# Performance work log

Hardware: AMD Instinct MI355X
Metric: run time of the kernel (lower is better)

Reference implementation:

```python
import jax, jax.numpy as jnp
from jax import lax
import numpy as np

N_TOTAL = 262144
NUM_SAMPLE = 1024
KNN_K = 16
NUM_CLASSES = 13
HIDDEN = 128
EPS = 1e-8


def _sqdist(a, b):
    # (Na,3),(Nb,3) -> (Na,Nb) squared euclidean; same argmin as torch.cdist
    return (jnp.sum(a * a, axis=1)[:, None]
            + jnp.sum(b * b, axis=1)[None, :]
            - 2.0 * a @ b.T)


def _farthest_point_sample(xyz, n_samples):
    # sequential FPS starting from index 0 (deterministic start)
    n = xyz.shape[0]

    def step(carry, _):
        min_d2, last = carry
        d2 = jnp.sum((xyz - xyz[last]) ** 2, axis=-1)
        min_d2 = jnp.minimum(min_d2, d2)
        nxt = jnp.argmax(min_d2).astype(jnp.int32)
        return (min_d2, nxt), nxt

    init = (jnp.full((n,), 1e10, dtype=xyz.dtype), jnp.int32(0))
    _, idxs = lax.scan(step, init, None, length=n_samples - 1)
    return jnp.concatenate([jnp.zeros((1,), jnp.int32), idxs])


def _compute_normals(pts, k):
    # PCA normal per point from its k nearest neighbors (self excluded)
    d2 = _sqdist(pts, pts)                      # (S,S), S=1024 -> small
    _, nbr_idx = lax.top_k(-d2, k + 1)
    nbr = pts[nbr_idx[:, 1:]]                   # (S,k,3)
    centered = nbr - jnp.mean(nbr, axis=1, keepdims=True)
    cov = jnp.einsum('ski,skj->sij', centered, centered) / (k - 1)
    _, eigvecs = jnp.linalg.eigh(cov)           # ascending eigenvalues
    normal = eigvecs[..., 0]                    # smallest-eigval eigenvector
    return normal / (jnp.linalg.norm(normal, axis=-1, keepdims=True) + EPS)


def _forward(gaussian_positions, gaussian_colors, W1, b1, W2, b2, W3, b3):
    sample_idx = _farthest_point_sample(gaussian_positions, NUM_SAMPLE)
    dxyz = gaussian_positions[sample_idx]       # (S,3)
    drgb = gaussian_colors[sample_idx]          # (S,3)
    dnrm = _compute_normals(dxyz, KNN_K)        # (S,3)
    feats = jnp.concatenate([dxyz, drgb, dnrm], axis=1)  # (S,9)

    # pointwise segmentation network (stand-in for PointNet++ get_model)
    h = jax.nn.relu(feats @ W1 + b1)
    h = jax.nn.relu(h @ W2 + b2)
    pred = h @ W3 + b3                          # (S, num_classes)

    feat_down = jax.nn.softmax(pred, axis=1)
    lbl_down = jnp.argmax(pred, axis=1)

    # 1-NN label propagation: streaming-min candidate (memory-bound)
    d2_full = _sqdist(gaussian_positions, dxyz)  # (N, S) ~ 1 GB
    nearest = jnp.argmin(d2_full, axis=1)
    return feat_down[nearest], lbl_down[nearest]


def setup_inputs() -> dict:
    key = jax.random.key(0)
    ks = jax.random.split(key, 8)
    pos = jax.random.normal(ks[0], (N_TOTAL, 3), jnp.float32)
    col = jax.random.uniform(ks[1], (N_TOTAL, 3), jnp.float32)
    W1 = jax.random.normal(ks[2], (9, HIDDEN), jnp.float32) / np.sqrt(9.0)
    b1 = jnp.zeros((HIDDEN,), jnp.float32)
    W2 = jax.random.normal(ks[3], (HIDDEN, HIDDEN), jnp.float32) / np.sqrt(HIDDEN)
    b2 = jnp.zeros((HIDDEN,), jnp.float32)
    W3 = jax.random.normal(ks[4], (HIDDEN, NUM_CLASSES), jnp.float32) / np.sqrt(HIDDEN)
    b3 = jnp.zeros((NUM_CLASSES,), jnp.float32)
    return {"gaussian_positions": pos, "gaussian_colors": col,
            "W1": W1, "b1": b1, "W2": W2, "b2": b2, "W3": W3, "b3": b3}


def reference(gaussian_positions, gaussian_colors, W1, b1, W2, b2, W3, b3):
    return _forward(gaussian_positions, gaussian_colors, W1, b1, W2, b2, W3, b3)
```

## Files before the change

### kernel.cpp

```cpp
#include <hip/hip_runtime.h>
#include <math.h>

#define N_TOTAL    262144
#define NUM_SAMPLE 1024
#define FPS_BLOCKS 64
#define FPS_THREADS 256
#define FPS_PPT (N_TOTAL / (FPS_BLOCKS * FPS_THREADS))
#define M_WAVE 8
#define POOL (FPS_BLOCKS * 4 * M_WAVE)
#define ENT_PER_T (POOL / FPS_THREADS)
#define SEL_CAP 1023

__device__ __forceinline__ float addrn(float a, float b) { return __fadd_rn(a, b); }
__device__ __forceinline__ float subrn(float a, float b) { return __fsub_rn(a, b); }
__device__ __forceinline__ float mulrn(float a, float b) { return __fmul_rn(a, b); }

__device__ __forceinline__ float d2rn(float ax, float ay, float az,
                                      float bx, float by, float bz) {
  float dx = subrn(ax, bx), dy = subrn(ay, by), dz = subrn(az, bz);
  return addrn(addrn(mulrn(dx, dx), mulrn(dy, dy)), mulrn(dz, dz));
}

__device__ __forceinline__ unsigned long long shflxor_u64(unsigned long long v, int mk) {
  return (unsigned long long)__shfl_xor((long long)v, mk, 64);
}

__device__ __forceinline__ float slapy2f(float x, float y) {
  float xa = fabsf(x), ya = fabsf(y);
  float w = fmaxf(xa, ya), z = fminf(xa, ya);
  if (z == 0.f) return w;
  float t = z / w;
  return w * __fsqrt_rn(1.f + t * t);
}

__device__ __forceinline__ void slartgf(float f, float g, float& c, float& s, float& r) {
  if (g == 0.f) { c = 1.f; s = 0.f; r = f; }
  else if (f == 0.f) { c = 0.f; s = (g > 0.f) ? 1.f : -1.f; r = fabsf(g); }
  else {
    float d = __fsqrt_rn(f * f + g * g);
    c = fabsf(f) / d;
    r = (f >= 0.f) ? d : -d;
    s = g / r;
  }
}

__device__ void slaev2f(float a, float b, float c0, float& rt1, float& rt2,
                        float& cs1, float& sn1) {
  float sm = a + c0, df = a - c0;
  float adf = fabsf(df), tb = b + b, ab = fabsf(tb);
  float acmx, acmn;
  if (fabsf(a) > fabsf(c0)) { acmx = a; acmn = c0; } else { acmx = c0; acmn = a; }
  float rt;
  if (adf > ab)      { float t = ab / adf; rt = adf * __fsqrt_rn(1.f + t * t); }
  else if (adf < ab) { float t = adf / ab; rt = ab * __fsqrt_rn(1.f + t * t); }
  else               { rt = ab * __fsqrt_rn(2.f); }
  int sgn1;
  if (sm < 0.f)      { rt1 = 0.5f * (sm - rt); sgn1 = -1; rt2 = (acmx / rt1) * acmn - (b / rt1) * b; }
  else if (sm > 0.f) { rt1 = 0.5f * (sm + rt); sgn1 = 1;  rt2 = (acmx / rt1) * acmn - (b / rt1) * b; }
  else               { rt1 = 0.5f * rt; rt2 = -0.5f * rt; sgn1 = 1; }
  float cs; int sgn2;
  if (df >= 0.f) { cs = df + rt; sgn2 = 1; } else { cs = df - rt; sgn2 = -1; }
  float acs = fabsf(cs);
  if (acs > ab) {
    float ct = -tb / cs;
    sn1 = 1.f / __fsqrt_rn(1.f + ct * ct);
    cs1 = ct * sn1;
  } else {
    if (ab == 0.f) { cs1 = 1.f; sn1 = 0.f; }
    else { float tn = -cs / tb; cs1 = 1.f / __fsqrt_rn(1.f + tn * tn); sn1 = tn * cs1; }
  }
  if (sgn1 == sgn2) { float tn = cs1; cs1 = -sn1; sn1 = tn; }
}

#define D_(i) d[(i)-1]
#define E_(i) e[(i)-1]

__device__ void ssteqr3(float d[3], float e[2], float Z[3][3]) {
  const float eps    = 5.9604645e-08f;
  const float eps2   = 3.5527137e-15f;
  const float safmin = 1.17549435e-38f;
  const float ssfmax = 3.0744573e+18f;
  const float ssfmin = 3.0517578e-05f;
  const int n = 3;
  int jtot = 0, nmaxit = 90;
  int l1 = 1;

  while (true) {
    if (l1 > n) break;
    if (l1 > 1) E_(l1 - 1) = 0.f;
    int m = n;
    for (int mm = l1; mm <= n - 1; ++mm) {
      float tst = fabsf(E_(mm));
      if (tst == 0.f) { m = mm; break; }
      if (tst <= (__fsqrt_rn(fabsf(D_(mm))) * __fsqrt_rn(fabsf(D_(mm + 1)))) * eps) {
        E_(mm) = 0.f; m = mm; break;
      }
    }
    int l = l1, lsv = l, lend = m, lendsv = m;
    l1 = m + 1;
    if (lend == l) continue;

    float anorm = fabsf(D_(lend));
    for (int i2 = l; i2 <= lend - 1; ++i2) {
      anorm = fmaxf(anorm, fabsf(D_(i2)));
      anorm = fmaxf(anorm, fabsf(E_(i2)));
    }
    int iscale = 0;
    if (anorm == 0.f) continue;
    if (anorm > ssfmax) {
      iscale = 1; float mul = ssfmax / anorm;
      for (int i2 = l; i2 <= lend; ++i2) D_(i2) *= mul;
      for (int i2 = l; i2 <= lend - 1; ++i2) E_(i2) *= mul;
    } else if (anorm < ssfmin) {
      iscale = 2; float mul = ssfmin / anorm;
      for (int i2 = l; i2 <= lend; ++i2) D_(i2) *= mul;
      for (int i2 = l; i2 <= lend - 1; ++i2) E_(i2) *= mul;
    }

    if (fabsf(D_(lend)) < fabsf(D_(l))) { int t = l; l = lend; lend = t; }

    if (lend > l) {
      while (true) {
        int m2 = lend;
        if (l != lend) {
          for (int mm = l; mm <= lend - 1; ++mm) {
            float tst = fabsf(E_(mm)); tst = tst * tst;
            if (tst <= (eps2 * fabsf(D_(mm))) * fabsf(D_(mm + 1)) + safmin) { m2 = mm; break; }
          }
        }
        if (m2 < lend) E_(m2) = 0.f;
        float p = D_(l);
        if (m2 == l) { D_(l) = p; l = l + 1; if (l <= lend) continue; break; }
        if (m2 == l + 1) {
          float rt1, rt2, cc, ss;
          slaev2f(D_(l), E_(l), D_(l + 1), rt1, rt2, cc, ss);
          for (int i2 = 0; i2 < 3; ++i2) {
            float tmp = Z[i2][l];
            Z[i2][l]     = cc * tmp - ss * Z[i2][l - 1];
            Z[i2][l - 1] = ss * tmp + cc * Z[i2][l - 1];
          }
          D_(l) = rt1; D_(l + 1) = rt2; E_(l) = 0.f;
          l = l + 2; if (l <= lend) continue; break;
        }
        if (jtot == nmaxit) break;
        ++jtot;
        float g = (D_(l + 1) - p) / (2.f * E_(l));
        float r = slapy2f(g, 1.f);
        float sgn_rg = (g >= 0.f) ? r : -r;
        g = D_(m2) - p + E_(l) / (g + sgn_rg);
        float s = 1.f, c = 1.f;
        p = 0.f;
        float csv[2], ssv[2];
        for (int i2 = m2 - 1; i2 >= l; --i2) {
          float f = s * E_(i2);
          float b = c * E_(i2);
          slartgf(g, f, c, s, r);
          if (i2 != m2 - 1) E_(i2 + 1) = r;
          g = D_(i2 + 1) - p;
          r = (D_(i2) - g) * s + 2.f * c * b;
          p = s * r;
          D_(i2 + 1) = g + p;
          g = c * r - b;
          csv[i2 - l] = c; ssv[i2 - l] = -s;
        }
        for (int j = m2 - 1; j >= l; --j) {
          float ct = csv[j - l], st = ssv[j - l];
          for (int i2 = 0; i2 < 3; ++i2) {
            float tmp = Z[i2][j];
            Z[i2][j]     = ct * tmp - st * Z[i2][j - 1];
            Z[i2][j - 1] = st * tmp + ct * Z[i2][j - 1];
          }
        }
        D_(l) = D_(l) - p;
        E_(l) = g;
      }
    } else {
      while (true) {
        int m2 = lend;
        if (l != lend) {
          for (int mm = l; mm >= lend + 1; --mm) {
            float tst = fabsf(E_(mm - 1)); tst = tst * tst;
            if (tst <= (eps2 * fabsf(D_(mm))) * fabsf(D_(mm - 1)) + safmin) { m2 = mm; break; }
          }
        }
        if (m2 > lend) E_(m2 - 1) = 0.f;
        float p = D_(l);
        if (m2 == l) { D_(l) = p; l = l - 1; if (l >= lend) continue; break; }
        if (m2 == l - 1) {
          float rt1, rt2, cc, ss;
          slaev2f(D_(l - 1), E_(l - 1), D_(l), rt1, rt2, cc, ss);
          for (int i2 = 0; i2 < 3; ++i2) {
            float tmp = Z[i2][l - 1];
            Z[i2][l - 1] = cc * tmp - ss * Z[i2][l - 2];
            Z[i2][l - 2] = ss * tmp + cc * Z[i2][l - 2];
          }
          D_(l - 1) = rt1; D_(l) = rt2; E_(l - 1) = 0.f;
          l = l - 2; if (l >= lend) continue; break;
        }
        if (jtot == nmaxit) break;
        ++jtot;
        float g = (D_(l - 1) - p) / (2.f * E_(l - 1));
        float r = slapy2f(g, 1.f);
        float sgn_rg = (g >= 0.f) ? r : -r;
        g = D_(m2) - p + E_(l - 1) / (g + sgn_rg);
        float s = 1.f, c = 1.f;
        p = 0.f;
        float csv[2], ssv[2];
        for (int i2 = m2; i2 <= l - 1; ++i2) {
          float f = s * E_(i2);
          float b = c * E_(i2);
          slartgf(g, f, c, s, r);
          if (i2 != m2) E_(i2 - 1) = r;
          g = D_(i2) - p;
          r = (D_(i2 + 1) - g) * s + 2.f * c * b;
          p = s * r;
          D_(i2) = g + p;
          g = c * r - b;
          csv[i2 - m2] = c; ssv[i2 - m2] = s;
        }
        for (int j = m2; j <= l - 1; ++j) {
          float ct = csv[j - m2], st = ssv[j - m2];
          for (int i2 = 0; i2 < 3; ++i2) {
            float tmp = Z[i2][j];
            Z[i2][j]     = ct * tmp - st * Z[i2][j - 1];
            Z[i2][j - 1] = st * tmp + ct * Z[i2][j - 1];
          }
        }
        D_(l) = D_(l) - p;
        E_(l - 1) = g;
      }
    }
    if (iscale == 1) {
      float mul = anorm / ssfmax;
      for (int i2 = lsv; i2 <= lendsv; ++i2) D_(i2) *= mul;
      for (int i2 = lsv; i2 <= lendsv - 1; ++i2) E_(i2) *= mul;
    } else if (iscale == 2) {
      float mul = anorm / ssfmin;
      for (int i2 = lsv; i2 <= lendsv; ++i2) D_(i2) *= mul;
      for (int i2 = lsv; i2 <= lendsv - 1; ++i2) E_(i2) *= mul;
    }
  }
  for (int ii = 2; ii <= n; ++ii) {
    int i2 = ii - 1, k = i2;
    float p = D_(i2);
    for (int j = ii; j <= n; ++j) if (D_(j) < p) { k = j; p = D_(j); }
    if (k != i2) {
      D_(k) = D_(i2); D_(i2) = p;
      for (int rr = 0; rr < 3; ++rr) {
        float t = Z[rr][i2 - 1]; Z[rr][i2 - 1] = Z[rr][k - 1]; Z[rr][k - 1] = t;
      }
    }
  }
}

__device__ void eigh3_smallest(float a00, float a10, float a20, float a11, float a21, float a22,
                               float& nx, float& ny, float& nz) {
  float d[3], e[2];
  float Z[3][3] = {{1.f,0.f,0.f},{0.f,1.f,0.f},{0.f,0.f,1.f}};
  float tau, v2;
  {
    float alpha = a10, x = a20;
    float xnorm = fabsf(x);
    if (xnorm == 0.f) {
      tau = 0.f; v2 = 0.f;
      d[0] = a00; d[1] = a11; d[2] = a22;
      e[0] = alpha; e[1] = a21;
    } else {
      float beta = -copysignf(slapy2f(alpha, x), alpha);
      tau = (beta - alpha) / beta;
      v2 = x / (alpha - beta);
      float w0 = (tau * a11) + tau * (a21 * v2);
      float w1 = (tau * a21) + (tau * v2) * a22;
      float ac = (-0.5f * tau) * (w0 + w1 * v2);
      w0 = w0 + ac;
      w1 = w1 + ac * v2;
      d[0] = a00;
      d[1] = (a11 - w0) - w0;
      d[2] = (a22 - v2 * w1) - w1 * v2;
      e[0] = beta;
      e[1] = (a21 - v2 * w0) - w1;
    }
  }
  ssteqr3(d, e, Z);
  if (tau != 0.f) {
    for (int c = 0; c < 3; ++c) {
      float w = Z[1][c] + Z[2][c] * v2;
      float temp = (-tau) * w;
      Z[1][c] = Z[1][c] + temp;
      Z[2][c] = Z[2][c] + v2 * temp;
    }
  }
  nx = Z[0][0]; ny = Z[1][0]; nz = Z[2][0];
}

__global__ void k0_init(unsigned long long* cand, int* sample_idx) {
  int t = blockIdx.x * blockDim.x + threadIdx.x;
  if (t < 2 * POOL) cand[t] = 0ull;
  if (t == 0) sample_idx[0] = 0;
}

__global__ __launch_bounds__(FPS_THREADS) void k1_fps(
    const float* __restrict__ pos,
    unsigned long long* __restrict__ cand,
    int* __restrict__ sample_idx) {
  __shared__ float pool_x[POOL], pool_y[POOL], pool_z[POOL];
  __shared__ float sel_x[SEL_CAP], sel_y[SEL_CAP], sel_z[SEL_CAP];
  __shared__ unsigned long long wb_key[2][4];
  __shared__ unsigned wb_ent[2][4];
  __shared__ unsigned long long tred[4];
  __shared__ int sh_selcnt;

  const int tidx = threadIdx.x;
  const int lane = tidx & 63, wv = tidx >> 6;
  const int gtid = blockIdx.x * FPS_THREADS + tidx;

  float px[FPS_PPT], py[FPS_PPT], pz[FPS_PPT], md[FPS_PPT];
#pragma unroll
  for (int k = 0; k < FPS_PPT; ++k) {
    int p = gtid + k * (FPS_BLOCKS * FPS_THREADS);
    px[k] = pos[3 * p]; py[k] = pos[3 * p + 1]; pz[k] = pos[3 * p + 2];
    md[k] = 1e10f;
  }
  const unsigned kbase = (unsigned)(0x3FFFFF - gtid) << 10;
  if (tidx == 0) { sel_x[0] = pos[0]; sel_y[0] = pos[1]; sel_z[0] = pos[2]; }
  __syncthreads();
  int sel_cnt = 1, total = 0, bt = 0;
  while (total < NUM_SAMPLE - 1) {
    ++bt;
    for (int s = 0; s < sel_cnt; ++s) {
      float lx = sel_x[s], ly = sel_y[s], lz = sel_z[s];
#pragma unroll
      for (int k = 0; k < FPS_PPT; ++k)
        md[k] = fminf(md[k], d2rn(px[k], py[k], pz[k], lx, ly, lz));
    }
    unsigned long long wkey[FPS_PPT];
#pragma unroll
    for (int k = 0; k < FPS_PPT; ++k)
      wkey[k] = ((unsigned long long)__float_as_uint(md[k]) << 32) |
                (unsigned long long)(kbase - ((unsigned)k << 24));
    unsigned long long mypub = 0ull;
    for (int r = 0; r < M_WAVE; ++r) {
      unsigned long long best = wkey[0];
#pragma unroll
      for (int k = 1; k < FPS_PPT; ++k) best = (wkey[k] > best) ? wkey[k] : best;
#pragma unroll
      for (int mk = 1; mk < 64; mk <<= 1) {
        unsigned long long o = shflxor_u64(best, mk);
        best = (o > best) ? o : best;
      }
      if (lane == r) mypub = best;
#pragma unroll
      for (int k = 0; k < FPS_PPT; ++k)
        if (wkey[k] == best) wkey[k] = 0ull;
    }
    const unsigned tag = (unsigned)bt & 1023u;
    unsigned long long* setbase = cand + (size_t)(bt & 1) * POOL;
    if (lane < M_WAVE)
      __hip_atomic_store(setbase + blockIdx.x * (4 * M_WAVE) + wv * M_WAVE + lane,
                         mypub | tag, __ATOMIC_RELAXED, __HIP_MEMORY_SCOPE_AGENT);
    const int base_w = tidx * ENT_PER_T;
    unsigned long long ckey[ENT_PER_T];
    {
      unsigned done = 0;
      while (done != 0xFFu) {
#pragma unroll
        for (int j = 0; j < ENT_PER_T; ++j) {
          if (!((done >> j) & 1u)) {
            unsigned long long v = __hip_atomic_load(setbase + base_w + j,
                                                     __ATOMIC_RELAXED, __HIP_MEMORY_SCOPE_AGENT);
            if ((unsigned)(v & 1023ull) == tag) { done |= 1u << j; ckey[j] = v & ~1023ull; }
          }
        }
        if (done != 0xFFu) __builtin_amdgcn_s_sleep(1);
      }
    }
    float cx[ENT_PER_T], cy[ENT_PER_T], cz[ENT_PER_T];
#pragma unroll
    for (int j = 0; j < ENT_PER_T; ++j) {
      int gidx = 0x3FFFFF - (int)((ckey[j] >> 10) & 0x3FFFFFull);
      cx[j] = pos[3 * gidx]; cy[j] = pos[3 * gidx + 1]; cz[j] = pos[3 * gidx + 2];
      pool_x[base_w + j] = cx[j]; pool_y[base_w + j] = cy[j]; pool_z[base_w + j] = cz[j];
    }
    {
      unsigned long long tb = ckey[ENT_PER_T - 1];
#pragma unroll
      for (int mk = 1; mk < 64; mk <<= 1) {
        unsigned long long o = shflxor_u64(tb, mk);
        tb = (o > tb) ? o : tb;
      }
      if (lane == 0) tred[wv] = tb;
    }
    __syncthreads();
    unsigned long long Tkey = tred[0];
#pragma unroll
    for (int w = 1; w < 4; ++w) Tkey = (tred[w] > Tkey) ? tred[w] : Tkey;
    int picks = 0;
    const int room = (NUM_SAMPLE - 1) - total;
    for (;;) {
      const int q = picks & 1;
      unsigned long long bk = ckey[0]; unsigned be = (unsigned)base_w;
#pragma unroll
      for (int j = 1; j < ENT_PER_T; ++j)
        if (ckey[j] > bk) { bk = ckey[j]; be = (unsigned)(base_w + j); }
#pragma unroll
      for (int mk = 1; mk < 64; mk <<= 1) {
        unsigned long long ok = shflxor_u64(bk, mk);
        unsigned oe = (unsigned)__shfl_xor((int)be, mk, 64);
        if (ok > bk) { bk = ok; be = oe; }
      }
      if (lane == 0) { wb_key[q][wv] = bk; wb_ent[q][wv] = be; }
      __syncthreads();
      unsigned long long gk = wb_key[q][0]; unsigned ge = wb_ent[q][0];
#pragma unroll
      for (int w = 1; w < 4; ++w)
        if (wb_key[q][w] > gk) { gk = wb_key[q][w]; ge = wb_ent[q][w]; }
      if (gk < Tkey || picks >= room) break;
      float Xp = pool_x[ge], Yp = pool_y[ge], Zp = pool_z[ge];
      if (tidx == 0) {
        sel_x[picks] = Xp; sel_y[picks] = Yp; sel_z[picks] = Zp;
        if (blockIdx.x == 0)
          sample_idx[1 + total + picks] = 0x3FFFFF - (int)((gk >> 10) & 0x3FFFFFull);
      }
#pragma unroll
      for (int j = 0; j < ENT_PER_T; ++j)
        if ((unsigned)(base_w + j) == ge) ckey[j] = 0ull;
#pragma unroll
      for (int j = 0; j < ENT_PER_T; ++j) {
        if (ckey[j]) {
          float d2 = d2rn(cx[j], cy[j], cz[j], Xp, Yp, Zp);
          unsigned long long nk = ((unsigned long long)__float_as_uint(d2) << 32) |
                                  (ckey[j] & 0xFFFFFFFFull);
          if (nk < ckey[j]) ckey[j] = nk;
        }
      }
      ++picks;
    }
    if (tidx == 0) sh_selcnt = picks;
    __syncthreads();
    sel_cnt = sh_selcnt;
    total += sel_cnt;
  }
}

__global__ __launch_bounds__(256) void k2a_knn(
    const float* __restrict__ pos, const float* __restrict__ col,
    const int* __restrict__ sample_idx,
    float4* __restrict__ sp4g, float* __restrict__ feats9) {
  __shared__ float4 sp[NUM_SAMPLE];
  const int tid = threadIdx.x, lane = tid & 63, wv = tid >> 6;
  for (int i = tid; i < NUM_SAMPLE; i += 256) {
    int idx = sample_idx[i];
    float x = pos[3 * idx], y = pos[3 * idx + 1], z = pos[3 * idx + 2];
    float nrm = addrn(addrn(mulrn(x, x), mulrn(y, y)), mulrn(z, z));
    float4 v = make_float4(x, y, z, nrm);
    sp[i] = v;
    if (blockIdx.x == 0) sp4g[i] = v;
  }
  __syncthreads();
  for (int it = 0; it < 4; ++it) {
    const int r = blockIdx.x * 16 + wv * 4 + it;
    float4 pr = sp[r];
    unsigned long long kk[16];
#pragma unroll
    for (int k = 0; k < 16; ++k) {
      int j = lane + 64 * k;
      float4 q = sp[j];
      float dot = fmaf(pr.z, q.z, fmaf(pr.y, q.y, mulrn(pr.x, q.x)));
      float d2 = subrn(addrn(pr.w, q.w), mulrn(2.f, dot));
      unsigned b = __float_as_uint(d2);
      unsigned sbits = (b & 0x80000000u) ? ~b : (b | 0x80000000u);
      kk[k] = ((unsigned long long)sbits << 32) | (unsigned)j;
    }
    int bi[17];
#pragma unroll
    for (int rsel = 0; rsel < 17; ++rsel) {
      unsigned long long best = 0xFFFFFFFFFFFFFFFFull;
#pragma unroll
      for (int k = 0; k < 16; ++k) best = (kk[k] < best) ? kk[k] : best;
#pragma unroll
      for (int mk = 1; mk < 64; mk <<= 1) {
        unsigned long long o = (unsigned long long)__shfl_xor((long long)best, mk, 64);
        best = (o < best) ? o : best;
      }
      int j = (int)(best & 0xFFFFFFFFull);
      bi[rsel] = j;
#pragma unroll
      for (int k = 0; k < 16; ++k)
        if (((j >> 6) == k) && ((j & 63) == lane)) kk[k] = 0xFFFFFFFFFFFFFFFFull;
    }
    float mx = 0.f, my = 0.f, mz = 0.f;
#pragma unroll
    for (int k = 1; k <= 16; ++k) {
      float4 q = sp[bi[k]];
      mx = addrn(mx, q.x); my = addrn(my, q.y); mz = addrn(mz, q.z);
    }
    mx = mulrn(mx, 0.0625f); my = mulrn(my, 0.0625f); mz = mulrn(mz, 0.0625f);
    float c00 = 0.f, c01 = 0.f, c02 = 0.f, c11 = 0.f, c12 = 0.f, c22 = 0.f;
#pragma unroll
    for (int k = 1; k <= 16; ++k) {
      float4 q = sp[bi[k]];
      float dx = subrn(q.x, mx), dy = subrn(q.y, my), dz = subrn(q.z, mz);
      c00 = addrn(c00, mulrn(dx, dx)); c01 = addrn(c01, mulrn(dx, dy));
      c02 = addrn(c02, mulrn(dx, dz)); c11 = addrn(c11, mulrn(dy, dy));
      c12 = addrn(c12, mulrn(dy, dz)); c22 = addrn(c22, mulrn(dz, dz));
    }
    c00 /= 15.f; c01 /= 15.f; c02 /= 15.f; c11 /= 15.f; c12 /= 15.f; c22 /= 15.f;

    float n0, n1, n2;
    eigh3_smallest(c00, c01, c02, c11, c12, c22, n0, n1, n2);
    float nn = __fsqrt_rn(addrn(addrn(mulrn(n0, n0), mulrn(n1, n1)), mulrn(n2, n2)));
    float den = addrn(nn, 1e-8f);
    n0 /= den; n1 /= den; n2 /= den;

    if (lane == 0) {
      int myidx = sample_idx[r];
      float* f = feats9 + r * 9;
      f[0] = pr.x; f[1] = pr.y; f[2] = pr.z;
      f[3] = col[3 * myidx]; f[4] = col[3 * myidx + 1]; f[5] = col[3 * myidx + 2];
      f[6] = n0; f[7] = n1; f[8] = n2;
    }
  }
}

__global__ __launch_bounds__(64) void k2b_mlp(
    const float* __restrict__ W1, const float* __restrict__ b1,
    const float* __restrict__ W2, const float* __restrict__ b2,
    const float* __restrict__ W3, const float* __restrict__ b3,
    const float* __restrict__ feats9,
    float* __restrict__ featd, int* __restrict__ lbl) {
  __shared__ float hbuf[64][129];
  const int tid = threadIdx.x;
  const int r = blockIdx.x * 64 + tid;
  float f9[9];
#pragma unroll
  for (int k = 0; k < 9; ++k) f9[k] = feats9[r * 9 + k];
  for (int jo = 0; jo < 128; ++jo) {
    float acc = 0.f;
#pragma unroll
    for (int k = 0; k < 9; ++k) acc = fmaf(f9[k], W1[k * 128 + jo], acc);
    acc += b1[jo];
    hbuf[tid][jo] = fmaxf(acc, 0.f);
  }
  float pd[13];
#pragma unroll
  for (int c = 0; c < 13; ++c) pd[c] = 0.f;
  for (int io = 0; io < 128; io += 16) {
    float acc[16];
#pragma unroll
    for (int t = 0; t < 16; ++t) acc[t] = 0.f;
    for (int j = 0; j < 128; ++j) {
      float hj = hbuf[tid][j];
#pragma unroll
      for (int t = 0; t < 16; ++t) acc[t] = fmaf(hj, W2[j * 128 + io + t], acc[t]);
    }
#pragma unroll
    for (int t = 0; t < 16; ++t) {
      float h2 = fmaxf(acc[t] + b2[io + t], 0.f);
#pragma unroll
      for (int c = 0; c < 13; ++c) pd[c] = fmaf(h2, W3[(io + t) * 13 + c], pd[c]);
    }
  }
#pragma unroll
  for (int c = 0; c < 13; ++c) pd[c] += b3[c];
  float mmax = pd[0];
#pragma unroll
  for (int c = 1; c < 13; ++c) mmax = fmaxf(mmax, pd[c]);
  float es = 0.f, ev[13];
#pragma unroll
  for (int c = 0; c < 13; ++c) { ev[c] = expf(pd[c] - mmax); es += ev[c]; }
#pragma unroll
  for (int c = 0; c < 13; ++c) featd[r * 13 + c] = ev[c] / es;
  int am = 0; float bv = pd[0];
#pragma unroll
  for (int c = 1; c < 13; ++c) { if (pd[c] > bv) { bv = pd[c]; am = c; } }
  lbl[r] = am;
}

__global__ __launch_bounds__(256) void k3_assign(
    const float* __restrict__ pos,
    const float4* __restrict__ sp4g,
    const float* __restrict__ featd,
    const int* __restrict__ lbl,
    float* __restrict__ out) {
  __shared__ float4 sp[NUM_SAMPLE];
  for (int i = threadIdx.x; i < NUM_SAMPLE; i += 256) sp[i] = sp4g[i];
  __syncthreads();
  int i = blockIdx.x * 256 + threadIdx.x;
  float x = pos[3 * i], y = pos[3 * i + 1], z = pos[3 * i + 2];
  float an = addrn(addrn(mulrn(x, x), mulrn(y, y)), mulrn(z, z));
  float bestd = 3.402823466e+38f; int bestj = 0;
#pragma unroll 4
  for (int j = 0; j < NUM_SAMPLE; ++j) {
    float4 q = sp[j];
    float dot = fmaf(z, q.z, fmaf(y, q.y, mulrn(x, q.x)));
    float d2 = subrn(addrn(an, q.w), mulrn(2.f, dot));
    if (d2 < bestd) { bestd = d2; bestj = j; }
  }
  const float* fr = featd + bestj * 13;
  float* o = out + (size_t)i * 13;
#pragma unroll
  for (int c = 0; c < 13; ++c) o[c] = fr[c];
  out[(size_t)N_TOTAL * 13 + i] = (float)lbl[bestj];
}

extern "C" void kernel_launch(void* const* d_in, const int* in_sizes, int n_in,
                              void* d_out, int out_size, void* d_ws, size_t ws_size,
                              hipStream_t stream) {
  (void)in_sizes; (void)n_in; (void)out_size; (void)ws_size;
  const float* pos = (const float*)d_in[0];
  const float* col = (const float*)d_in[1];
  const float* W1 = (const float*)d_in[2];
  const float* b1 = (const float*)d_in[3];
  const float* W2 = (const float*)d_in[4];
  const float* b2 = (const float*)d_in[5];
  const float* W3 = (const float*)d_in[6];
  const float* b3 = (const float*)d_in[7];
  float* out = (float*)d_out;

  char* w = (char*)d_ws;
  unsigned long long* cand = (unsigned long long*)(w);
  int* sample_idx = (int*)(w + 65536);
  float4* sp4g = (float4*)(w + 73728);
  float* featd = (float*)(w + 90112);
  int* lbl = (int*)(w + 143360);
  float* feats9 = (float*)(w + 147456);

  k0_init<<<16, 256, 0, stream>>>(cand, sample_idx);
  k1_fps<<<FPS_BLOCKS, FPS_THREADS, 0, stream>>>(pos, cand, sample_idx);
  k2a_knn<<<64, 256, 0, stream>>>(pos, col, sample_idx, sp4g, feats9);
  k2b_mlp<<<16, 64, 0, stream>>>(W1, b1, W2, b2, W3, b3, feats9, featd, lbl);
  k3_assign<<<N_TOTAL / 256, 256, 0, stream>>>(pos, sp4g, featd, lbl, out);
}
```

Measured before the change: 2.049 ms.

## Replace 64-bit shuffle argmax reductions with DPP float/uint two-pass reductions in FPS

After: 1.931 ms. 5.7% less time.

```diff
diff --git a/kernel.cpp b/kernel.cpp
--- a/kernel.cpp
+++ b/kernel.cpp
@@ -21,8 +21,28 @@
   return addrn(addrn(mulrn(dx, dx), mulrn(dy, dy)), mulrn(dz, dz));
 }
 
-__device__ __forceinline__ unsigned long long shflxor_u64(unsigned long long v, int mk) {
-  return (unsigned long long)__shfl_xor((long long)v, mk, 64);
+template <int CTRL>
+__device__ __forceinline__ int dpp_i(int x) {
+  return __builtin_amdgcn_update_dpp(x, x, CTRL, 0xF, 0xF, false);
+}
+__device__ __forceinline__ float wave_fmax_bcast(float v) {
+  v = fmaxf(v, __int_as_float(dpp_i<0x111>(__float_as_int(v))));
+  v = fmaxf(v, __int_as_float(dpp_i<0x112>(__float_as_int(v))));
+  v = fmaxf(v, __int_as_float(dpp_i<0x114>(__float_as_int(v))));
+  v = fmaxf(v, __int_as_float(dpp_i<0x118>(__float_as_int(v))));
+  v = fmaxf(v, __int_as_float(dpp_i<0x142>(__float_as_int(v))));
+  v = fmaxf(v, __int_as_float(dpp_i<0x143>(__float_as_int(v))));
+  return __int_as_float(__builtin_amdgcn_readlane(__float_as_int(v), 63));
+}
+__device__ __forceinline__ unsigned wave_umax_bcast(unsigned v) {
+  unsigned o;
+  o = (unsigned)dpp_i<0x111>((int)v); v = (o > v) ? o : v;
+  o = (unsigned)dpp_i<0x112>((int)v); v = (o > v) ? o : v;
+  o = (unsigned)dpp_i<0x114>((int)v); v = (o > v) ? o : v;
+  o = (unsigned)dpp_i<0x118>((int)v); v = (o > v) ? o : v;
+  o = (unsigned)dpp_i<0x142>((int)v); v = (o > v) ? o : v;
+  o = (unsigned)dpp_i<0x143>((int)v); v = (o > v) ? o : v;
+  return (unsigned)__builtin_amdgcn_readlane((int)v, 63);
 }
 
 __device__ __forceinline__ float slapy2f(float x, float y) {
@@ -303,11 +323,11 @@
     const float* __restrict__ pos,
     unsigned long long* __restrict__ cand,
     int* __restrict__ sample_idx) {
-  __shared__ float pool_x[POOL], pool_y[POOL], pool_z[POOL];
   __shared__ float sel_x[SEL_CAP], sel_y[SEL_CAP], sel_z[SEL_CAP];
-  __shared__ unsigned long long wb_key[2][4];
-  __shared__ unsigned wb_ent[2][4];
-  __shared__ unsigned long long tred[4];
+  __shared__ float wb_md[2][4], wb_x[2][4], wb_y[2][4], wb_z[2][4];
+  __shared__ unsigned wb_idf[2][4];
+  __shared__ float tred_md[4];
+  __shared__ unsigned tred_idf[4];
   __shared__ int sh_selcnt;
 
   const int tidx = threadIdx.x;
@@ -321,7 +341,7 @@
     px[k] = pos[3 * p]; py[k] = pos[3 * p + 1]; pz[k] = pos[3 * p + 2];
     md[k] = 1e10f;
   }
-  const unsigned kbase = (unsigned)(0x3FFFFF - gtid) << 10;
+  const unsigned idf0 = 0x3FFFFFu - (unsigned)gtid;
   if (tidx == 0) { sel_x[0] = pos[0]; sel_y[0] = pos[1]; sel_z[0] = pos[2]; }
   __syncthreads();
   int sel_cnt = 1, total = 0, bt = 0;
@@ -333,33 +353,38 @@
       for (int k = 0; k < FPS_PPT; ++k)
         md[k] = fminf(md[k], d2rn(px[k], py[k], pz[k], lx, ly, lz));
     }
-    unsigned long long wkey[FPS_PPT];
-#pragma unroll
-    for (int k = 0; k < FPS_PPT; ++k)
-      wkey[k] = ((unsigned long long)__float_as_uint(md[k]) << 32) |
-                (unsigned long long)(kbase - ((unsigned)k << 24));
-    unsigned long long mypub = 0ull;
-    for (int r = 0; r < M_WAVE; ++r) {
-      unsigned long long best = wkey[0];
-#pragma unroll
-      for (int k = 1; k < FPS_PPT; ++k) best = (wkey[k] > best) ? wkey[k] : best;
-#pragma unroll
-      for (int mk = 1; mk < 64; mk <<= 1) {
-        unsigned long long o = shflxor_u64(best, mk);
-        best = (o > best) ? o : best;
-      }
-      if (lane == r) mypub = best;
-#pragma unroll
-      for (int k = 0; k < FPS_PPT; ++k)
-        if (wkey[k] == best) wkey[k] = 0ull;
-    }
     const unsigned tag = (unsigned)bt & 1023u;
     unsigned long long* setbase = cand + (size_t)(bt & 1) * POOL;
-    if (lane < M_WAVE)
-      __hip_atomic_store(setbase + blockIdx.x * (4 * M_WAVE) + wv * M_WAVE + lane,
-                         mypub | tag, __ATOMIC_RELAXED, __HIP_MEMORY_SCOPE_AGENT);
+    {
+      float wmd[FPS_PPT];
+#pragma unroll
+      for (int k = 0; k < FPS_PPT; ++k) wmd[k] = md[k];
+      unsigned long long mypub = 0ull;
+      for (int r = 0; r < M_WAVE; ++r) {
+        float bm = wmd[0]; unsigned bidf = idf0;
+#pragma unroll
+        for (int k = 1; k < FPS_PPT; ++k) {
+          unsigned idfk = idf0 - ((unsigned)k << 14);
+          if (wmd[k] > bm || (wmd[k] == bm && idfk > bidf)) { bm = wmd[k]; bidf = idfk; }
+        }
+        float wmx = wave_fmax_bcast(bm);
+        unsigned tb = (bm == wmx) ? bidf : 0u;
+        unsigned widf = wave_umax_bcast(tb);
+        if (lane == r)
+          mypub = ((unsigned long long)__float_as_uint(wmx) << 32) |
+                  ((unsigned long long)widf << 10);
+#pragma unroll
+        for (int k = 0; k < FPS_PPT; ++k) {
+          unsigned idfk = idf0 - ((unsigned)k << 14);
+          if (wmd[k] == wmx && idfk == widf) wmd[k] = -1.f;
+        }
+      }
+      if (lane < M_WAVE)
+        __hip_atomic_store(setbase + blockIdx.x * (4 * M_WAVE) + wv * M_WAVE + lane,
+                           mypub | tag, __ATOMIC_RELAXED, __HIP_MEMORY_SCOPE_AGENT);
+    }
     const int base_w = tidx * ENT_PER_T;
-    unsigned long long ckey[ENT_PER_T];
+    float cmd[ENT_PER_T]; unsigned cidf[ENT_PER_T];
     {
       unsigned done = 0;
       while (done != 0xFFu) {
@@ -368,7 +393,11 @@
           if (!((done >> j) & 1u)) {
             unsigned long long v = __hip_atomic_load(setbase + base_w + j,
                                                      __ATOMIC_RELAXED, __HIP_MEMORY_SCOPE_AGENT);
-            if ((unsigned)(v & 1023ull) == tag) { done |= 1u << j; ckey[j] = v & ~1023ull; }
+            if ((unsigned)(v & 1023ull) == tag) {
+              done |= 1u << j;
+              cmd[j] = __uint_as_float((unsigned)(v >> 32));
+              cidf[j] = (unsigned)((v >> 10) & 0x3FFFFFull);
+            }
           }
         }
         if (done != 0xFFu) __builtin_amdgcn_s_sleep(1);
@@ -377,61 +406,56 @@
     float cx[ENT_PER_T], cy[ENT_PER_T], cz[ENT_PER_T];
 #pragma unroll
     for (int j = 0; j < ENT_PER_T; ++j) {
-      int gidx = 0x3FFFFF - (int)((ckey[j] >> 10) & 0x3FFFFFull);
+      int gidx = 0x3FFFFF - (int)cidf[j];
       cx[j] = pos[3 * gidx]; cy[j] = pos[3 * gidx + 1]; cz[j] = pos[3 * gidx + 2];
-      pool_x[base_w + j] = cx[j]; pool_y[base_w + j] = cy[j]; pool_z[base_w + j] = cz[j];
     }
     {
-      unsigned long long tb = ckey[ENT_PER_T - 1];
-#pragma unroll
-      for (int mk = 1; mk < 64; mk <<= 1) {
-        unsigned long long o = shflxor_u64(tb, mk);
-        tb = (o > tb) ? o : tb;
-      }
-      if (lane == 0) tred[wv] = tb;
+      float t7 = cmd[ENT_PER_T - 1]; unsigned t7i = cidf[ENT_PER_T - 1];
+      float twm = wave_fmax_bcast(t7);
+      unsigned ttb = (t7 == twm) ? t7i : 0u;
+      unsigned twi = wave_umax_bcast(ttb);
+      if (lane == 0) { tred_md[wv] = twm; tred_idf[wv] = twi; }
     }
     __syncthreads();
-    unsigned long long Tkey = tred[0];
-#pragma unroll
-    for (int w = 1; w < 4; ++w) Tkey = (tred[w] > Tkey) ? tred[w] : Tkey;
+    float Tmd = tred_md[0]; unsigned Tidf = tred_idf[0];
+#pragma unroll
+    for (int w = 1; w < 4; ++w) {
+      float m2 = tred_md[w]; unsigned i2v = tred_idf[w];
+      if (m2 > Tmd || (m2 == Tmd && i2v > Tidf)) { Tmd = m2; Tidf = i2v; }
+    }
     int picks = 0;
     const int room = (NUM_SAMPLE - 1) - total;
     for (;;) {
       const int q = picks & 1;
-      unsigned long long bk = ckey[0]; unsigned be = (unsigned)base_w;
+      float bm = cmd[0]; unsigned bidf = cidf[0]; int bj = 0;
 #pragma unroll
       for (int j = 1; j < ENT_PER_T; ++j)
-        if (ckey[j] > bk) { bk = ckey[j]; be = (unsigned)(base_w + j); }
-#pragma unroll
-      for (int mk = 1; mk < 64; mk <<= 1) {
-        unsigned long long ok = shflxor_u64(bk, mk);
-        unsigned oe = (unsigned)__shfl_xor((int)be, mk, 64);
-        if (ok > bk) { bk = ok; be = oe; }
-      }
-      if (lane == 0) { wb_key[q][wv] = bk; wb_ent[q][wv] = be; }
+        if (cmd[j] > bm || (cmd[j] == bm && cidf[j] > bidf)) { bm = cmd[j]; bidf = cidf[j]; bj = j; }
+      float wmx = wave_fmax_bcast(bm);
+      unsigned tb = (bm == wmx) ? bidf : 0u;
+      unsigned widf = wave_umax_bcast(tb);
+      if (bm == wmx && bidf == widf) {
+        wb_md[q][wv] = wmx; wb_idf[q][wv] = widf;
+        wb_x[q][wv] = cx[bj]; wb_y[q][wv] = cy[bj]; wb_z[q][wv] = cz[bj];
+      }
       __syncthreads();
-      unsigned long long gk = wb_key[q][0]; unsigned ge = wb_ent[q][0];
-#pragma unroll
-      for (int w = 1; w < 4; ++w)
-        if (wb_key[q][w] > gk) { gk = wb_key[q][w]; ge = wb_ent[q][w]; }
-      if (gk < Tkey || picks >= room) break;
-      float Xp = pool_x[ge], Yp = pool_y[ge], Zp = pool_z[ge];
+      float gm = wb_md[q][0]; unsigned gi = wb_idf[q][0]; int gw = 0;
+#pragma unroll
+      for (int w = 1; w < 4; ++w) {
+        float m2 = wb_md[q][w]; unsigned i2v = wb_idf[q][w];
+        if (m2 > gm || (m2 == gm && i2v > gi)) { gm = m2; gi = i2v; gw = w; }
+      }
+      if ((gm < Tmd || (gm == Tmd && gi < Tidf)) || picks >= room) break;
+      float Xp = wb_x[q][gw], Yp = wb_y[q][gw], Zp = wb_z[q][gw];
       if (tidx == 0) {
         sel_x[picks] = Xp; sel_y[picks] = Yp; sel_z[picks] = Zp;
-        if (blockIdx.x == 0)
-          sample_idx[1 + total + picks] = 0x3FFFFF - (int)((gk >> 10) & 0x3FFFFFull);
-      }
-#pragma unroll
-      for (int j = 0; j < ENT_PER_T; ++j)
-        if ((unsigned)(base_w + j) == ge) ckey[j] = 0ull;
+        if (blockIdx.x == 0) sample_idx[1 + total + picks] = 0x3FFFFF - (int)gi;
+      }
 #pragma unroll
       for (int j = 0; j < ENT_PER_T; ++j) {
-        if (ckey[j]) {
-          float d2 = d2rn(cx[j], cy[j], cz[j], Xp, Yp, Zp);
-          unsigned long long nk = ((unsigned long long)__float_as_uint(d2) << 32) |
-                                  (ckey[j] & 0xFFFFFFFFull);
-          if (nk < ckey[j]) ckey[j] = nk;
-        }
+        if (cmd[j] == gm && cidf[j] == gi) cmd[j] = -1.f;
+        float d2 = d2rn(cx[j], cy[j], cz[j], Xp, Yp, Zp);
+        if (d2 < cmd[j]) cmd[j] = d2;
       }
       ++picks;
     }
```
